# Optimization experiments

Hardware: AMD Instinct MI355X
Metric: run time of the kernel (lower is better)

The kernel has to match this reference:

```python
import jax, jax.numpy as jnp
import numpy as np

V, D_EMB, H = 50000, 200, 150
NC, NA, NT = 119, 103, 11
B, T = 32, 512
LC, LV = 50, 50
EC, EA = 600, 500


def setup_inputs() -> dict:
    key = jax.random.key(0)
    ks = iter(jax.random.split(key, 64))
    nrm = lambda shape, s=1.0: jax.random.normal(next(ks), shape, jnp.float32) * s
    rint = lambda shape, hi: jax.random.randint(next(ks), shape, 0, hi, jnp.int32)
    inp = {}
    inp['E'] = nrm((V, D_EMB), 0.1)
    inp['charge_tokens'] = rint((NC, LC), V)
    inp['article_tokens'] = rint((NA, LC), V)
    inp['documents'] = rint((B, T), V)
    inp['charge_verdict_tokens'] = rint((NC, LV), V)
    inp['article_verdict_tokens'] = rint((NA, LV), V)
    inp['c_src'] = rint((EC,), NC); inp['c_dst'] = rint((EC,), NC)
    inp['a_src'] = rint((EA,), NA); inp['a_dst'] = rint((EA,), NA)
    for nm, (i_d, h_d) in [('enc', (D_EMB, H)), ('encch', (D_EMB, H)),
                           ('term', (6 * H, 3 * H)), ('art', (8 * H, 4 * H))]:
        inp[nm + '_Wih'] = nrm((2, 3 * h_d, i_d), 1.0 / np.sqrt(i_d))
        inp[nm + '_Whh'] = nrm((2, 3 * h_d, h_d), 1.0 / np.sqrt(h_d))
        inp[nm + '_bih'] = nrm((2, 3 * h_d), 0.01)
        inp[nm + '_bhh'] = nrm((2, 3 * h_d), 0.01)
    inp['W_charge'] = nrm((NC, 6 * H), 0.05); inp['b_charge'] = nrm((NC,), 0.01)
    inp['W_article'] = nrm((NA, 8 * H), 0.05); inp['b_article'] = nrm((NA,), 0.01)
    inp['W_time'] = nrm((NT, 6 * H), 0.05); inp['b_time'] = nrm((NT,), 0.01)
    return inp


def _gru_dir(x, Wih, Whh, bih, bhh, reverse):
    # x: [B, T, I] -> outputs [B, T, H]; PyTorch GRU gate order (r, z, n)
    Bb = x.shape[0]
    Hh = Whh.shape[1]
    xs = jnp.einsum('bti,gi->btg', x, Wih) + bih  # [B,T,3H]
    if reverse:
        xs = xs[:, ::-1]
    def step(h, xt):
        gh = h @ Whh.T + bhh
        xr, xz, xn = jnp.split(xt, 3, axis=-1)
        hr, hz, hn = jnp.split(gh, 3, axis=-1)
        r = jax.nn.sigmoid(xr + hr)
        z = jax.nn.sigmoid(xz + hz)
        n = jnp.tanh(xn + r * hn)
        h = (1.0 - z) * n + z * h
        return h, h
    h0 = jnp.zeros((Bb, Hh), x.dtype)
    _, ys = jax.lax.scan(step, h0, jnp.swapaxes(xs, 0, 1))
    ys = jnp.swapaxes(ys, 0, 1)
    if reverse:
        ys = ys[:, ::-1]
    return ys


def bigru(x, Wih, Whh, bih, bhh):
    f = _gru_dir(x, Wih[0], Whh[0], bih[0], bhh[0], False)
    b = _gru_dir(x, Wih[1], Whh[1], bih[1], bhh[1], True)
    return jnp.concatenate([f, b], axis=-1)


def graph_decomp(L, src, dst, n, layers=2):
    # ragged neighbor-weighted label-graph decomposition, CSR-style via segment_sum
    counts = jax.ops.segment_sum(jnp.ones(src.shape, L.dtype), src, num_segments=n)
    for _ in range(layers):
        Li, Lj = L[src], L[dst]
        coef = (Li * Lj).sum(-1) / ((Lj * Lj).sum(-1) + 1e-10)
        agg = jax.ops.segment_sum(coef[:, None] * Lj, src, num_segments=n)
        mean = agg / jnp.maximum(counts, 1.0)[:, None]
        L = jnp.where((counts > 0)[:, None], L - mean, L)
    return L


def code_wise(query, context):
    # query [B,N,D], context [B,T,D] -> [B,D]
    S = jnp.einsum('btd,bnd->btn', context, query)
    att = jax.nn.softmax(S.max(-1), axis=-1)  # [B,T]
    return jnp.einsum('bt,btd->bd', att, context)


def mask_att(query, context):
    # query [B,Tv,D], context [B,Tc,D] -> [B,Tc,D]
    att = jnp.einsum('btd,bvd->btv', context, query)
    masked = jnp.where(att == 0, -jnp.inf, att)
    p = jax.nn.softmax(masked, axis=-1)
    p = jnp.where(jnp.isnan(p), 0.0, p)
    return jnp.einsum('btv,bvd->btd', p, query)


def fact_sep(E, verd_table, pred, enc, circumstance):
    verdict = E[verd_table[pred]]            # [B, LV, D_EMB]
    vh = bigru(verdict, *enc)                # [B, LV, 300]
    scenario = mask_att(vh, circumstance)    # [B, T, 300]
    x3 = (circumstance * scenario).sum(-1)
    x4 = (scenario * scenario).sum(-1) + 1e-10
    similar = (x3 / x4)[..., None] * scenario
    return similar, circumstance - similar


def _tile(v, t):
    return jnp.broadcast_to(v[:, None, :], (v.shape[0], t, v.shape[1]))


def reference(E, charge_tokens, article_tokens, documents, charge_verdict_tokens,
              article_verdict_tokens, c_src, c_dst, a_src, a_dst,
              enc_Wih, enc_Whh, enc_bih, enc_bhh,
              encch_Wih, encch_Whh, encch_bih, encch_bhh,
              term_Wih, term_Whh, term_bih, term_bhh,
              art_Wih, art_Whh, art_bih, art_bhh,
              W_charge, b_charge, W_article, b_article, W_time, b_time):
    enc = (enc_Wih, enc_Whh, enc_bih, enc_bhh)
    encch = (encch_Wih, encch_Whh, encch_bih, encch_bhh)
    enc_term = (term_Wih, term_Whh, term_bih, term_bhh)
    enc_art = (art_Wih, art_Whh, art_bih, art_bhh)

    ch_h = bigru(E[charge_tokens], *encch)    # [NC, LC, 300]
    ar_h = bigru(E[article_tokens], *encch)   # [NA, LC, 300]
    _charge = ch_h.mean(1)
    _article = ar_h.mean(1)
    ori_a, ori_b = _charge, _article
    new_charge = graph_decomp(_charge, c_src, c_dst, NC, 2)
    new_article = graph_decomp(_article, a_src, a_dst, NA, 2)

    d_hidden = bigru(E[documents], *enc)      # [B, T, 300]
    Bb, Tt, Dd = d_hidden.shape

    q_c = jnp.broadcast_to(new_charge[None], (Bb,) + new_charge.shape)
    d_hidden_charge = _tile(code_wise(q_c, d_hidden), Tt)
    q_a = jnp.broadcast_to(ori_a[None], (Bb,) + ori_a.shape)
    d_a = _tile(code_wise(q_a, d_hidden), Tt)

    fact_charge = jnp.concatenate([d_hidden, d_hidden_charge, d_a], -1)  # [B,T,900]
    df = fact_charge.mean(1)
    charge_out = df @ W_charge.T + b_charge

    c_pred = jnp.argmax(charge_out, axis=1)
    adc_vector, sec_vector = fact_sep(E, charge_verdict_tokens, c_pred, enc, d_hidden)

    q_na = jnp.broadcast_to(new_article[None], (Bb,) + new_article.shape)
    d_hidden_article = _tile(code_wise(q_na, d_hidden), Tt)
    q_b = jnp.broadcast_to(ori_b[None], (Bb,) + ori_b.shape)
    d_b = _tile(code_wise(q_b, d_hidden), Tt)

    fact_article = jnp.concatenate([d_hidden, d_hidden_article, adc_vector, d_b], -1)  # [B,T,1200]
    fa_h = bigru(fact_article, *enc_art)
    article_out = fa_h.mean(1) @ W_article.T + b_article

    a_pred = jnp.argmax(article_out, axis=1)
    ssc_vector, dsc_vector = fact_sep(E, article_verdict_tokens, a_pred, enc, sec_vector)

    term = jnp.concatenate([d_hidden, ssc_vector, dsc_vector], -1)  # [B,T,900]
    th = bigru(term, *enc_term)
    time_out = th.mean(1) @ W_time.T + b_time
    return (charge_out, article_out, time_out)
```

## Files before the change

### kernel.cpp

```cpp
#include <hip/hip_runtime.h>
#include <stdint.h>
#include <math.h>

typedef unsigned int u32;
typedef unsigned long long u64;
typedef _Float16 f16;
typedef _Float16 h4 __attribute__((ext_vector_type(4)));
typedef _Float16 h2 __attribute__((ext_vector_type(2)));
typedef _Float16 h8 __attribute__((ext_vector_type(8)));
typedef float f4 __attribute__((ext_vector_type(4)));

#define Vn     50000
#define DEMBn  200
#define Hn     150
#define NCn    119
#define NAn    103
#define NTn    11
#define Bn     32
#define Tn     512
#define LCn    50
#define LVn    50
#define ECn    600
#define EAn    500

#define IDIV 1073741824

__device__ __forceinline__ float sigm(float x){ return 1.0f / (1.0f + expf(-x)); }

#if __has_builtin(__builtin_amdgcn_fdot2)
__device__ __forceinline__ float FDOT2(h2 a, h2 b, float c){
  return __builtin_amdgcn_fdot2(a, b, c, false);
}
#else
__device__ __forceinline__ float FDOT2(h2 a, h2 b, float c){
  return c + (float)a.x*(float)b.x + (float)a.y*(float)b.y;
}
#endif

__device__ __forceinline__ u64 llc_load64(const u64* p){
  return __hip_atomic_load(p, __ATOMIC_RELAXED, __HIP_MEMORY_SCOPE_AGENT);
}
__device__ __forceinline__ void llc_store64(u64* p, u64 v){
  __hip_atomic_store(p, v, __ATOMIC_RELAXED, __HIP_MEMORY_SCOPE_AGENT);
}

template<int AMODE>
__global__ __launch_bounds__(256)
void gemm_k(const float* A0, const float* A1, const float* A2,
            const float* Etab, const int* tok,
            const float* Bm, int ldb, int bc0, int bc1, int bc2,
            const float* bias, const float* rowbias, int rb_div, int rb_stride,
            int arow_div, int arow_stride, int arow_off,
            float* C, int M, int N, int K)
{
  __shared__ float As[8][132];
  __shared__ float Bs[8][132];
  __shared__ int tokS[128];
  int tid = threadIdx.x;
  int m0 = blockIdx.y * 128, n0 = blockIdx.x * 128;
  if (AMODE == 1){
    for (int i = tid; i < 128; i += 256){
      int m = m0 + i;
      tokS[i] = (m < M) ? tok[m] : 0;
    }
  }
  __syncthreads();
  float acc[8][8];
  #pragma unroll
  for (int i=0;i<8;i++)
    #pragma unroll
    for (int j=0;j<8;j++) acc[i][j] = 0.f;

  int tx = tid & 15, ty = tid >> 4;

  for (int k0 = 0; k0 < K; k0 += 8){
    #pragma unroll
    for (int r = 0; r < 4; r++){
      int i = tid + 256*r;
      int ml = i >> 3, kl = i & 7;
      int k = k0 + kl;
      {
        int m = m0 + ml;
        float v = 0.f;
        if (m < M && k < K){
          if (AMODE == 0){
            int s = k / 300; int kk = k - s*300;
            const float* Ap = (s==0) ? A0 : ((s==1) ? A1 : A2);
            int ar = (m / arow_div)*arow_stride + (m % arow_div) + arow_off;
            v = Ap[(size_t)ar*300 + kk];
          } else {
            v = Etab[(size_t)tokS[ml]*DEMBn + k];
          }
        }
        As[kl][ml] = v;
      }
      {
        int n = n0 + ml;
        float v = 0.f;
        if (n < N && k < K){
          int col;
          if (AMODE == 0){ int s = k / 300; int kk = k - s*300; col = ((s==0)?bc0:((s==1)?bc1:bc2)) + kk; }
          else col = k;
          v = Bm[(size_t)n*ldb + col];
        }
        Bs[kl][ml] = v;
      }
    }
    __syncthreads();
    #pragma unroll
    for (int kk = 0; kk < 8; kk++){
      float a[8], b[8];
      #pragma unroll
      for (int i=0;i<8;i++) a[i] = As[kk][ty*8+i];
      #pragma unroll
      for (int i=0;i<8;i++) b[i] = Bs[kk][tx*8+i];
      #pragma unroll
      for (int i=0;i<8;i++)
        #pragma unroll
        for (int j=0;j<8;j++) acc[i][j] += a[i]*b[j];
    }
    __syncthreads();
  }
  #pragma unroll
  for (int i=0;i<8;i++){
    int m = m0 + ty*8 + i; if (m >= M) continue;
    #pragma unroll
    for (int j=0;j<8;j++){
      int n = n0 + tx*8 + j; if (n >= N) continue;
      float v = acc[i][j];
      if (bias)    v += bias[n];
      if (rowbias) v += rowbias[(size_t)(m / rb_div)*rb_stride + n];
      C[(size_t)m*N + n] = v;
    }
  }
}

__global__ __launch_bounds__(256)
void score_rowmax_k(const float* A, const float* Bq, int Nq, float* RMX)
{
  __shared__ float As[8][132];
  __shared__ float Bs[8][132];
  int tid = threadIdx.x;
  int m0 = blockIdx.x * 128;
  float acc[8][8];
  #pragma unroll
  for (int i=0;i<8;i++)
    #pragma unroll
    for (int j=0;j<8;j++) acc[i][j] = 0.f;
  int tx = tid & 15, ty = tid >> 4;

  for (int k0 = 0; k0 < 300; k0 += 8){
    #pragma unroll
    for (int r = 0; r < 4; r++){
      int i = tid + 256*r;
      int ml = i >> 3, kl = i & 7;
      int k = k0 + kl;
      As[kl][ml] = (k < 300) ? A[(size_t)(m0 + ml)*300 + k] : 0.f;
      Bs[kl][ml] = (ml < Nq && k < 300) ? Bq[(size_t)ml*300 + k] : 0.f;
    }
    __syncthreads();
    #pragma unroll
    for (int kk = 0; kk < 8; kk++){
      float a[8], b[8];
      #pragma unroll
      for (int i=0;i<8;i++) a[i] = As[kk][ty*8+i];
      #pragma unroll
      for (int i=0;i<8;i++) b[i] = Bs[kk][tx*8+i];
      #pragma unroll
      for (int i=0;i<8;i++)
        #pragma unroll
        for (int j=0;j<8;j++) acc[i][j] += a[i]*b[j];
    }
    __syncthreads();
  }
  #pragma unroll
  for (int i=0;i<8;i++){
    float mx = -INFINITY;
    #pragma unroll
    for (int j=0;j<8;j++){
      int n = tx*8 + j;
      if (n < Nq) mx = fmaxf(mx, acc[i][j]);
    }
    mx = fmaxf(mx, __shfl_xor(mx, 1));
    mx = fmaxf(mx, __shfl_xor(mx, 2));
    mx = fmaxf(mx, __shfl_xor(mx, 4));
    mx = fmaxf(mx, __shfl_xor(mx, 8));
    if (tx == 0) RMX[m0 + ty*8 + i] = mx;
  }
}

__global__ __launch_bounds__(256)
void stage_mfma_k(const float* A0, const float* A1, const float* A2,
                  const float* Bm, int ldb, int bc0, int bc1, int bc2,
                  const float* bias, const float* rowbias, int rb_stride,
                  int arow_off,
                  float* C, int N, int K)
{
  constexpr int KP = 40;
  __shared__ __align__(16) f16 Ah[128*KP];
  __shared__ __align__(16) f16 Al[128*KP];
  __shared__ __align__(16) f16 Bh[128*KP];
  __shared__ __align__(16) f16 Bl[128*KP];

  int tid = threadIdx.x;
  int n0 = blockIdx.x * 128, m0 = blockIdx.y * 128;
  int lane = tid & 63, w = tid >> 6;
  int wr = (w >> 1) * 64, wc = (w & 1) * 64;
  int li = lane & 15, lk = (lane >> 4) * 8;

  f4 acc[4][4];
  #pragma unroll
  for (int i=0;i<4;i++)
    #pragma unroll
    for (int j=0;j<4;j++) acc[i][j] = (f4){0.f,0.f,0.f,0.f};

  int srow = tid >> 1, scb = (tid & 1) << 4;
  int sm = m0 + srow;
  size_t abase = (size_t)(((sm >> 8) * 512) + (sm & 255) + arow_off) * 300;
  int sn = n0 + srow;

  for (int k0 = 0; k0 < K; k0 += 32){
    #pragma unroll
    for (int q = 0; q < 16; q += 2){
      float2 va = {0.f, 0.f}, vb = {0.f, 0.f};
      int k = k0 + scb + q;
      if (k < K){
        int s = (k >= 600) ? 2 : ((k >= 300) ? 1 : 0);
        int kk = k - s*300;
        const float* Ap = (s==0) ? A0 : ((s==1) ? A1 : A2);
        va = *(const float2*)&Ap[abase + kk];
        if (sn < N) vb = *(const float2*)&Bm[(size_t)sn*ldb + ((s==0)?bc0:((s==1)?bc1:bc2)) + kk];
      }
      f16 a0h=(f16)va.x, a1h=(f16)va.y, b0h=(f16)vb.x, b1h=(f16)vb.y;
      f16 a0l=(f16)(va.x-(float)a0h), a1l=(f16)(va.y-(float)a1h);
      f16 b0l=(f16)(vb.x-(float)b0h), b1l=(f16)(vb.y-(float)b1h);
      int off = srow*KP + scb + q;
      *(h2*)&Ah[off] = (h2){a0h, a1h};
      *(h2*)&Al[off] = (h2){a0l, a1l};
      *(h2*)&Bh[off] = (h2){b0h, b1h};
      *(h2*)&Bl[off] = (h2){b0l, b1l};
    }
    __syncthreads();

    h8 fah[4], fal[4], fbh[4], fbl[4];
    #pragma unroll
    for (int f = 0; f < 4; f++){
      fah[f] = *(const h8*)&Ah[(wr + f*16 + li)*KP + lk];
      fal[f] = *(const h8*)&Al[(wr + f*16 + li)*KP + lk];
      fbh[f] = *(const h8*)&Bh[(wc + f*16 + li)*KP + lk];
      fbl[f] = *(const h8*)&Bl[(wc + f*16 + li)*KP + lk];
    }
    #pragma unroll
    for (int i = 0; i < 4; i++)
      #pragma unroll
      for (int j = 0; j < 4; j++){
        acc[i][j] = __builtin_amdgcn_mfma_f32_16x16x32_f16(fah[i], fbh[j], acc[i][j], 0,0,0);
        acc[i][j] = __builtin_amdgcn_mfma_f32_16x16x32_f16(fah[i], fbl[j], acc[i][j], 0,0,0);
        acc[i][j] = __builtin_amdgcn_mfma_f32_16x16x32_f16(fal[i], fbh[j], acc[i][j], 0,0,0);
      }
    __syncthreads();
  }

  #pragma unroll
  for (int i = 0; i < 4; i++){
    int r0 = m0 + wr + i*16 + (lane >> 4)*4;
    #pragma unroll
    for (int j = 0; j < 4; j++){
      int c = n0 + wc + j*16 + li;
      if (c < N){
        float badd = bias ? bias[c] : 0.f;
        #pragma unroll
        for (int r = 0; r < 4; r++){
          int row = r0 + r;
          float v = acc[i][j][r] + badd;
          if (rowbias) v += rowbias[(size_t)(row >> 8)*rb_stride + c];
          C[(size_t)row*N + c] = v;
        }
      }
    }
  }
}

__global__ __launch_bounds__(256)
void embed_mfma_k(const float* Etab, const int* tok,
                  const float* Bm, const float* bias,
                  float* C, int M, int N, int K)
{
  constexpr int KP = 40;
  __shared__ __align__(16) f16 Ah[128*KP];
  __shared__ __align__(16) f16 Al[128*KP];
  __shared__ __align__(16) f16 Bh[128*KP];
  __shared__ __align__(16) f16 Bl[128*KP];
  __shared__ int tokS[128];

  int tid = threadIdx.x;
  int n0 = blockIdx.x * 128, m0 = blockIdx.y * 128;
  int lane = tid & 63, w = tid >> 6;
  int wr = (w >> 1) * 64, wc = (w & 1) * 64;
  int li = lane & 15, lk = (lane >> 4) * 8;

  for (int i = tid; i < 128; i += 256){
    int m = m0 + i;
    tokS[i] = (m < M) ? tok[m] : 0;
  }
  __syncthreads();

  f4 acc[4][4];
  #pragma unroll
  for (int i=0;i<4;i++)
    #pragma unroll
    for (int j=0;j<4;j++) acc[i][j] = (f4){0.f,0.f,0.f,0.f};

  int srow = tid >> 1, scb = (tid & 1) << 4;
  size_t abase = (size_t)tokS[srow] * (size_t)K;
  int sn = n0 + srow;

  for (int k0 = 0; k0 < K; k0 += 32){
    #pragma unroll
    for (int q = 0; q < 16; q += 2){
      float2 va = {0.f, 0.f}, vb = {0.f, 0.f};
      int k = k0 + scb + q;
      if (k < K){
        va = *(const float2*)&Etab[abase + k];
        if (sn < N) vb = *(const float2*)&Bm[(size_t)sn*K + k];
      }
      f16 a0h=(f16)va.x, a1h=(f16)va.y, b0h=(f16)vb.x, b1h=(f16)vb.y;
      f16 a0l=(f16)(va.x-(float)a0h), a1l=(f16)(va.y-(float)a1h);
      f16 b0l=(f16)(vb.x-(float)b0h), b1l=(f16)(vb.y-(float)b1h);
      int off = srow*KP + scb + q;
      *(h2*)&Ah[off] = (h2){a0h, a1h};
      *(h2*)&Al[off] = (h2){a0l, a1l};
      *(h2*)&Bh[off] = (h2){b0h, b1h};
      *(h2*)&Bl[off] = (h2){b0l, b1l};
    }
    __syncthreads();

    h8 fah[4], fal[4], fbh[4], fbl[4];
    #pragma unroll
    for (int f = 0; f < 4; f++){
      fah[f] = *(const h8*)&Ah[(wr + f*16 + li)*KP + lk];
      fal[f] = *(const h8*)&Al[(wr + f*16 + li)*KP + lk];
      fbh[f] = *(const h8*)&Bh[(wc + f*16 + li)*KP + lk];
      fbl[f] = *(const h8*)&Bl[(wc + f*16 + li)*KP + lk];
    }
    #pragma unroll
    for (int i = 0; i < 4; i++)
      #pragma unroll
      for (int j = 0; j < 4; j++){
        acc[i][j] = __builtin_amdgcn_mfma_f32_16x16x32_f16(fah[i], fbh[j], acc[i][j], 0,0,0);
        acc[i][j] = __builtin_amdgcn_mfma_f32_16x16x32_f16(fah[i], fbl[j], acc[i][j], 0,0,0);
        acc[i][j] = __builtin_amdgcn_mfma_f32_16x16x32_f16(fal[i], fbh[j], acc[i][j], 0,0,0);
      }
    __syncthreads();
  }

  #pragma unroll
  for (int i = 0; i < 4; i++){
    int r0 = m0 + wr + i*16 + (lane >> 4)*4;
    #pragma unroll
    for (int j = 0; j < 4; j++){
      int c = n0 + wc + j*16 + li;
      if (c < N){
        float badd = bias ? bias[c] : 0.f;
        #pragma unroll
        for (int r = 0; r < 4; r++){
          int row = r0 + r;
          if (row < M) C[(size_t)row*N + c] = acc[i][j][r] + badd;
        }
      }
    }
  }
}

__global__ __launch_bounds__(640)
void gru_small_k(const float* xs, int ncols,
                 const float* Whh, const float* bhh,
                 float* ys, float* meanOut, int T)
{
  constexpr int KSTEP = 38;
  __shared__ __align__(16) float hl[2][152];
  int tid = threadIdx.x;
  int seq = blockIdx.x, dir = blockIdx.y;
  int row = tid >> 2, l = tid & 3;
  bool comp = (row < 150);
  int k0 = l * KSTEP;

  float w0[KSTEP], w1[KSTEP], w2[KSTEP];
  if (comp){
    const float* base = Whh + (size_t)dir*67500;
    const float* p0 = base + (size_t)(0*150 + row)*150;
    const float* p1 = base + (size_t)(1*150 + row)*150;
    const float* p2 = base + (size_t)(2*150 + row)*150;
    #pragma unroll
    for (int i=0;i<KSTEP;i++){
      int k = k0 + i;
      int kc = (k < 150) ? k : 0;
      float m = (k < 150) ? 1.f : 0.f;
      w0[i] = p0[kc]*m; w1[i] = p1[kc]*m; w2[i] = p2[kc]*m;
    }
  }
  float bR=0.f, bZ=0.f, bN=0.f;
  if (comp && l==0){
    bR = bhh[dir*450 + row];
    bZ = bhh[dir*450 + 150 + row];
    bN = bhh[dir*450 + 300 + row];
  }
  for (int i = tid; i < 2*152; i += 640) (&hl[0][0])[i] = 0.f;
  __syncthreads();

  float msum = 0.f;
  size_t rowbase = (size_t)seq * T;
  for (int tt = 0; tt < T; tt++){
    int t = dir ? (T-1-tt) : tt;
    int par = tt & 1;
    const float* hr = hl[par];
    float* hw = hl[1-par];

    float xr=0.f, xz=0.f, xn=0.f, hprev=0.f;
    if (comp && l==0){
      const float* xp = xs + (rowbase + t)*(size_t)ncols + dir*450;
      xr = xp[row]; xz = xp[150+row]; xn = xp[300+row];
      hprev = hr[row];
    }

    float a0=0.f, a1=0.f, a2=0.f;
    if (comp){
      #pragma unroll
      for (int i=0;i<KSTEP;i++){
        float hv = hr[k0 + i];
        a0 += w0[i]*hv; a1 += w1[i]*hv; a2 += w2[i]*hv;
      }
    }
    a0 += __shfl_xor(a0,1); a0 += __shfl_xor(a0,2);
    a1 += __shfl_xor(a1,1); a1 += __shfl_xor(a1,2);
    a2 += __shfl_xor(a2,1); a2 += __shfl_xor(a2,2);

    if (comp && l==0){
      float rr = sigm(xr + a0 + bR);
      float zz = sigm(xz + a1 + bZ);
      float nn = tanhf(xn + rr*(a2 + bN));
      float hn = (1.f - zz)*nn + zz*hprev;
      hw[row] = hn;
      msum += hn;
      if (ys) ys[(rowbase + t)*(size_t)300 + dir*150 + row] = hn;
    }
    __syncthreads();
  }
  if (meanOut && comp && l==0)
    meanOut[(size_t)seq*300 + dir*150 + row] = msum / (float)T;
}

template<int BLK, int JB, int KC, int Hh>
__global__ __launch_bounds__(BLK)
void gru_big_k(const float* xs0, const float* xs1,
               const float* Whh,
               const float* bhh,
               u64* hbuf,
               float* hseed,
               float* meanOut, int mean_stride,
               u32 tagbase,
               int TT, int TC, int t0)
{
  constexpr int LPR   = 8;
  constexpr int KSTEP = 2*KC;
  constexpr int HS    = LPR*KSTEP;
  constexpr int HP    = Hh/2;
  constexpr int NPAIR = 4*HP;
  constexpr int RMAX  = (NPAIR + BLK - 1)/BLK;
  constexpr int H3    = 3*Hh;

  __shared__ __align__(16) f16 hstage[2][4*HS];

  int tid = threadIdx.x;
  int jc = blockIdx.x, bg = blockIdx.y, dir = blockIdx.z;
  int j0 = jc * JB;
  int row = tid >> 3, l = tid & 7;
  bool comp = (row < JB);
  int jg = j0 + row;
  int k0 = l * KSTEP;

  const float* Wd = Whh + (size_t)dir*H3*Hh;
  const float* xs = dir ? xs1 : xs0;
  int xoff = dir ? (TT - TC - t0) : t0;

  h2 w0[KC], w1[KC], w2[KC];
  if (comp){
    const float* p0 = Wd + ((size_t)0*Hh + jg)*(size_t)Hh;
    const float* p1 = Wd + ((size_t)1*Hh + jg)*(size_t)Hh;
    const float* p2 = Wd + ((size_t)2*Hh + jg)*(size_t)Hh;
    #pragma unroll
    for (int i=0;i<KC;i++){
      int k = k0 + 2*i;
      h2 a; a.x=(f16)0.f; a.y=(f16)0.f;
      h2 b = a, c = a;
      if (k < Hh){   a.x=(f16)p0[k];   b.x=(f16)p1[k];   c.x=(f16)p2[k]; }
      if (k+1 < Hh){ a.y=(f16)p0[k+1]; b.y=(f16)p1[k+1]; c.y=(f16)p2[k+1]; }
      w0[i]=a; w1[i]=b; w2[i]=c;
    }
  } else {
    #pragma unroll
    for (int i=0;i<KC;i++){
      h2 z; z.x=(f16)0.f; z.y=(f16)0.f;
      w0[i]=z; w1[i]=z; w2[i]=z;
    }
  }
  float br=0.f, bz=0.f, bn_=0.f;
  if (comp && l < 4){
    br = bhh[(size_t)dir*H3 + jg];
    bz = bhh[(size_t)dir*H3 + Hh + jg];
    bn_= bhh[(size_t)dir*H3 + 2*Hh + jg];
  }

  {
    f16* hz = &hstage[0][0];
    for (int i = tid; i < 2*4*HS; i += BLK) hz[i] = (f16)0.f;
  }

  float msum_own = 0.f;
  float hold_own = 0.f;
  if (t0 > 0 && comp && l < 4){
    const float* hs = hseed + (size_t)dir*Bn*Hh;
    hold_own = hs[(size_t)(bg*4+l)*Hh + jg];
  }
  __syncthreads();

  for (int tt = 0; tt < TC; tt++){
    int g = t0 + tt;
    int t = dir ? (TT-1-g) : g;
    int par = g & 1;
    const u64* hrd = hbuf + (size_t)(par*2 + dir)*Bn*HP;
    u64*       hwr = hbuf + (size_t)((1-par)*2 + dir)*Bn*HP;
    f16* hsb = hstage[par];

    u64 tmp[RMAX];
    const u64* hb = hrd + (size_t)(bg*4)*HP;
    if (g != 0){
      #pragma unroll
      for (int r=0;r<RMAX;r++){
        int idx = tid + r*BLK;
        if (idx < NPAIR) tmp[r] = llc_load64(&hb[idx]);
      }
    }

    float xr=0.f, xz=0.f, xn=0.f;
    if (comp && l < 4){
      const float* xp = xs + ((size_t)(bg*4+l)*TC + (t - xoff))*(size_t)H3;
      xr = xp[jg]; xz = xp[Hh+jg]; xn = xp[2*Hh+jg];
    }

    if (g != 0){
      u32 want = tagbase + (u32)g;
      u32 pend = 0;
      #pragma unroll
      for (int r=0;r<RMAX;r++){
        int idx = tid + r*BLK;
        if (idx < NPAIR && (u32)(tmp[r] >> 32) != want) pend |= (1u << r);
      }
      int guard = 0;
      while (pend){
        __builtin_amdgcn_s_sleep(1);
        #pragma unroll
        for (int r=0;r<RMAX;r++)
          if (pend & (1u << r)) tmp[r] = llc_load64(&hb[tid + r*BLK]);
        #pragma unroll
        for (int r=0;r<RMAX;r++)
          if ((pend & (1u << r)) && (u32)(tmp[r] >> 32) == want) pend &= ~(1u << r);
        if (++guard > 200000) break;
      }
      #pragma unroll
      for (int r=0;r<RMAX;r++){
        int idx = tid + r*BLK;
        if (idx < NPAIR){
          int s = idx / HP, jp = idx - s*HP;
          union { u32 i; h2 h; } u; u.i = (u32)tmp[r];
          *(h2*)(hsb + s*HS + 2*jp) = u.h;
        }
      }
    }
    __syncthreads();

    float a0[4]={0,0,0,0}, a1[4]={0,0,0,0}, a2[4]={0,0,0,0};
    if (comp){
      const f16* hp = hsb + k0;
      #pragma unroll
      for (int i=0;i<KC;i++){
        const int kk = 2*i;
        h2 hv0 = *(const h2*)(hp + 0*HS + kk);
        h2 hv1 = *(const h2*)(hp + 1*HS + kk);
        h2 hv2 = *(const h2*)(hp + 2*HS + kk);
        h2 hv3 = *(const h2*)(hp + 3*HS + kk);
        a0[0]=FDOT2(w0[i],hv0,a0[0]); a0[1]=FDOT2(w0[i],hv1,a0[1]);
        a0[2]=FDOT2(w0[i],hv2,a0[2]); a0[3]=FDOT2(w0[i],hv3,a0[3]);
        a1[0]=FDOT2(w1[i],hv0,a1[0]); a1[1]=FDOT2(w1[i],hv1,a1[1]);
        a1[2]=FDOT2(w1[i],hv2,a1[2]); a1[3]=FDOT2(w1[i],hv3,a1[3]);
        a2[0]=FDOT2(w2[i],hv0,a2[0]); a2[1]=FDOT2(w2[i],hv1,a2[1]);
        a2[2]=FDOT2(w2[i],hv2,a2[2]); a2[3]=FDOT2(w2[i],hv3,a2[3]);
      }
    }
    #pragma unroll
    for (int s=0;s<4;s++){
      a0[s] += __shfl_xor(a0[s],1); a0[s] += __shfl_xor(a0[s],2); a0[s] += __shfl_xor(a0[s],4);
      a1[s] += __shfl_xor(a1[s],1); a1[s] += __shfl_xor(a1[s],2); a1[s] += __shfl_xor(a1[s],4);
      a2[s] += __shfl_xor(a2[s],1); a2[s] += __shfl_xor(a2[s],2); a2[s] += __shfl_xor(a2[s],4);
    }
    float t0a = (l & 1) ? a0[1] : a0[0], t0b = (l & 1) ? a0[3] : a0[2];
    float A0 = (l & 2) ? t0b : t0a;
    float t1a = (l & 1) ? a1[1] : a1[0], t1b = (l & 1) ? a1[3] : a1[2];
    float A1 = (l & 2) ? t1b : t1a;
    float t2a = (l & 1) ? a2[1] : a2[0], t2b = (l & 1) ? a2[3] : a2[2];
    float A2 = (l & 2) ? t2b : t2a;

    float hn_own = 0.f;
    if (comp && l < 4){
      float rr = sigm(xr + A0 + br);
      float zz = sigm(xz + A1 + bz);
      float nn = tanhf(xn + rr*(A2 + bn_));
      hn_own = (1.f - zz)*nn + zz*hold_own;
      hold_own = hn_own;
      msum_own += hn_own;
    }
    u32 wtag = tagbase + (u32)g + 1u;
    float hp2 = __shfl_down(hn_own, 8);
    if (comp && l < 4 && !(row & 1)){
      h2 pk; pk.x = (f16)hn_own; pk.y = (f16)hp2;
      union { h2 h; u32 i; } u; u.h = pk;
      llc_store64(&hwr[(size_t)(bg*4+l)*HP + ((unsigned)(j0+row) >> 1)],
                  ((u64)wtag << 32) | (u64)u.i);
    }
    if (tt == TC-1 && comp && l < 4){
      float* hs = hseed + (size_t)dir*Bn*Hh;
      hs[(size_t)(bg*4+l)*Hh + jg] = hold_own;
    }
  }
  if (comp && l < 4){
    float* mp = meanOut + (size_t)(bg*4+l)*mean_stride + dir*Hh + jg;
    *mp += msum_own / (float)TT;
  }
}

__global__ __launch_bounds__(256)
void mask_att_k(const float* ctx, const float* vh, float* simOut, float* diffOut)
{
  __shared__ __align__(16) float vhl[50*300];
  __shared__ __align__(16) float ctxl[8*300];
  __shared__ float attl[8*52];
  __shared__ __align__(16) float scenl[8*300];
  __shared__ float ratio[8];
  int tid = threadIdx.x;
  int b = blockIdx.y, tc = blockIdx.x;
  int grp = tid >> 5, ln = tid & 31;
  size_t cbase = ((size_t)b*Tn + tc*8) * 300;
  {
    const f4* vsrc = (const f4*)(vh + (size_t)b*15000);
    f4* vdst = (f4*)vhl;
    for (int i = tid; i < 3750; i += 256) vdst[i] = vsrc[i];
    const f4* csrc = (const f4*)(ctx + cbase);
    f4* cdst = (f4*)ctxl;
    for (int i = tid; i < 600; i += 256) cdst[i] = csrc[i];
  }
  __syncthreads();
  for (int p = tid; p < 400; p += 256){
    int ttl = p / 50, v = p % 50;
    const f4* cp = (const f4*)(ctxl + ttl*300);
    const f4* vp = (const f4*)(vhl + v*300);
    float acc = 0.f;
    for (int d4 = 0; d4 < 75; d4++){
      f4 c = cp[d4], vv = vp[d4];
      acc += c.x*vv.x + c.y*vv.y + c.z*vv.z + c.w*vv.w;
    }
    attl[ttl*52 + v] = acc;
  }
  __syncthreads();
  {
    float mx = -INFINITY;
    for (int v = ln; v < 50; v += 32){
      float a = attl[grp*52+v];
      float msk = (a == 0.f) ? -INFINITY : a;
      attl[grp*52+v] = msk;
      mx = fmaxf(mx, msk);
    }
    #pragma unroll
    for (int m=1; m<32; m<<=1) mx = fmaxf(mx, __shfl_xor(mx, m));
    if (mx == -INFINITY){
      for (int v = ln; v < 50; v += 32) attl[grp*52+v] = 0.f;
    } else {
      float sum = 0.f;
      for (int v = ln; v < 50; v += 32){
        float e = expf(attl[grp*52+v] - mx);
        attl[grp*52+v] = e;
        sum += e;
      }
      #pragma unroll
      for (int m=1; m<32; m<<=1) sum += __shfl_xor(sum, m);
      float inv = 1.f/sum;
      for (int v = ln; v < 50; v += 32) attl[grp*52+v] *= inv;
    }
  }
  __syncthreads();
  for (int p = tid; p < 2400; p += 256){
    int ttl = p / 300, d = p % 300;
    float acc = 0.f;
    for (int v=0; v<50; v++) acc += attl[ttl*52+v] * vhl[v*300+d];
    scenl[p] = acc;
  }
  __syncthreads();
  {
    float x3 = 0.f, x4 = 0.f;
    for (int d = ln; d < 300; d += 32){
      float s = scenl[grp*300+d];
      x3 += ctxl[grp*300+d]*s; x4 += s*s;
    }
    #pragma unroll
    for (int m=1; m<32; m<<=1){ x3 += __shfl_xor(x3, m); x4 += __shfl_xor(x4, m); }
    if (ln == 0) ratio[grp] = x3 / (x4 + 1e-10f);
  }
  __syncthreads();
  {
    f4* so = (f4*)(simOut + cbase);
    f4* dfo = (f4*)(diffOut + cbase);
    const f4* sc = (const f4*)scenl;
    const f4* cl = (const f4*)ctxl;
    for (int p4 = tid; p4 < 600; p4 += 256){
      float rt = ratio[p4 / 75];
      f4 s = sc[p4], c = cl[p4];
      f4 sim = (f4){rt*s.x, rt*s.y, rt*s.z, rt*s.w};
      so[p4] = sim;
      dfo[p4] = (f4){c.x - sim.x, c.y - sim.y, c.z - sim.z, c.w - sim.w};
    }
  }
}

__global__ __launch_bounds__(256)
void softmaxT_k(const float* m, float* att){
  __shared__ float red[256];
  int b = blockIdx.x, tid = threadIdx.x;
  float v1 = m[b*512 + tid], v2 = m[b*512 + 256 + tid];
  red[tid] = fmaxf(v1, v2); __syncthreads();
  for (int s=128; s; s>>=1){ if (tid<s) red[tid] = fmaxf(red[tid], red[tid+s]); __syncthreads(); }
  float M = red[0]; __syncthreads();
  float e1 = expf(v1-M), e2 = expf(v2-M);
  red[tid] = e1+e2; __syncthreads();
  for (int s=128; s; s>>=1){ if (tid<s) red[tid] += red[tid+s]; __syncthreads(); }
  float inv = 1.f / red[0];
  att[b*512+tid] = e1*inv; att[b*512+256+tid] = e2*inv;
}

__global__ __launch_bounds__(256)
void wsum_k(const float* att, const float* dh, float* out){
  int b = blockIdx.x, c = blockIdx.y, tid = threadIdx.x;
  int t0 = c * 64;
  for (int d = tid; d < 300; d += 256){
    float acc = 0.f;
    #pragma unroll 8
    for (int t = t0; t < t0 + 64; t++)
      acc += att[b*512+t] * dh[((size_t)b*512 + t)*300 + d];
    atomicAdd(&out[b*300+d], acc);
  }
}

__global__ void count_k(const int* src, int E, float* counts){
  int e = blockIdx.x*256 + threadIdx.x;
  if (e < E) atomicAdd(&counts[src[e]], 1.f);
}
__global__ void coef_k(const float* L, const int* src, const int* dst, int E, float* coef){
  int e = blockIdx.x*4 + (threadIdx.x >> 6);
  int lane = threadIdx.x & 63;
  if (e >= E) return;
  const float* Li = L + (size_t)src[e]*300;
  const float* Lj = L + (size_t)dst[e]*300;
  float num = 0.f, den = 0.f;
  for (int d = lane; d < 300; d += 64){ float lj = Lj[d]; num += Li[d]*lj; den += lj*lj; }
  for (int off = 32; off; off >>= 1){ num += __shfl_xor(num, off, 64); den += __shfl_xor(den, off, 64); }
  if (lane == 0) coef[e] = num / (den + 1e-10f);
}
__global__ void agg_k(const float* L, const int* src, const int* dst, const float* coef, int E, float* agg){
  int e = blockIdx.x;
  float c = coef[e];
  const float* Lj = L + (size_t)dst[e]*300;
  float* ag = agg + (size_t)src[e]*300;
  for (int d = threadIdx.x; d < 300; d += 256) atomicAdd(&ag[d], c*Lj[d]);
}
__global__ void upd_k(const float* L, const float* agg, const float* counts, float* out, int n){
  int i = blockIdx.x;
  float c = counts[i];
  for (int d = threadIdx.x; d < 300; d += 256){
    float v = L[(size_t)i*300+d];
    out[(size_t)i*300+d] = (c > 0.f) ? v - agg[(size_t)i*300+d]/fmaxf(c, 1.f) : v;
  }
}

__global__ __launch_bounds__(256)
void logits_k(const float* A0, const float* A1, const float* A2, int srcw,
              const float* W, const float* bias, int C, int K,
              float* outF){
  int b = blockIdx.x;
  int c = blockIdx.y*4 + (threadIdx.x >> 6);
  int lane = threadIdx.x & 63;
  if (c >= C) return;
  const float* wp = W + (size_t)c*K;
  float acc = 0.f;
  for (int k = lane; k < K; k += 64){
    int s = k / srcw; int kk = k - s*srcw;
    const float* Ap = (s==0) ? A0 : ((s==1) ? A1 : A2);
    acc += Ap[(size_t)b*srcw + kk] * wp[k];
  }
  for (int off = 32; off; off >>= 1) acc += __shfl_xor(acc, off, 64);
  if (lane == 0) outF[b*C + c] = acc + bias[c];
}
__global__ void argmax_k(const float* lf, int C, int* pred){
  int b = threadIdx.x;
  if (b < 32){
    const float* p = lf + (size_t)b*C;
    int best = 0; float bv = p[0];
    for (int c = 1; c < C; c++){ float v = p[c]; if (v > bv){ bv = v; best = c; } }
    pred[b] = best;
  }
}
__global__ void vtok_k(const int* table, const int* pred, int* vt, int L){
  int i = blockIdx.x*256 + threadIdx.x;
  if (i < 32*L) vt[i] = table[pred[i/L]*L + i%L];
}

extern "C" void kernel_launch(void* const* d_in, const int* in_sizes, int n_in,
                              void* d_out, int out_size, void* d_ws, size_t ws_size,
                              hipStream_t stream)
{
  (void)in_sizes; (void)n_in; (void)out_size;
  const float* E        = (const float*)d_in[0];
  const int* chTok    = (const int*)d_in[1];
  const int* arTok    = (const int*)d_in[2];
  const int* docs     = (const int*)d_in[3];
  const int* chVerd   = (const int*)d_in[4];
  const int* arVerd   = (const int*)d_in[5];
  const int* c_src    = (const int*)d_in[6];
  const int* c_dst    = (const int*)d_in[7];
  const int* a_src    = (const int*)d_in[8];
  const int* a_dst    = (const int*)d_in[9];
  const float* enc_Wih  = (const float*)d_in[10];
  const float* enc_Whh  = (const float*)d_in[11];
  const float* enc_bih  = (const float*)d_in[12];
  const float* enc_bhh  = (const float*)d_in[13];
  const float* ech_Wih  = (const float*)d_in[14];
  const float* ech_Whh  = (const float*)d_in[15];
  const float* ech_bih  = (const float*)d_in[16];
  const float* ech_bhh  = (const float*)d_in[17];
  const float* term_Wih = (const float*)d_in[18];
  const float* term_Whh = (const float*)d_in[19];
  const float* term_bih = (const float*)d_in[20];
  const float* term_bhh = (const float*)d_in[21];
  const float* art_Wih  = (const float*)d_in[22];
  const float* art_Whh  = (const float*)d_in[23];
  const float* art_bih  = (const float*)d_in[24];
  const float* art_bhh  = (const float*)d_in[25];
  const float* W_charge = (const float*)d_in[26];
  const float* b_charge = (const float*)d_in[27];
  const float* W_article= (const float*)d_in[28];
  const float* b_article= (const float*)d_in[29];
  const float* W_time   = (const float*)d_in[30];
  const float* b_time   = (const float*)d_in[31];
  float* out = (float*)d_out;
  float* OUTC = out;
  float* OUTA = out + 3808;
  float* OUTT = out + 7104;

  char* wsb = (char*)d_ws;
  size_t off = 0;
  auto alloc = [&](size_t nf)->float* {
    float* p = (float*)(wsb + off);
    off += ((nf*4 + 255) & ~(size_t)255);
    return p;
  };
  float* XS0   = alloc(14745600ULL);
  float* XS1   = alloc(14745600ULL);
  float* DH    = alloc(4915200);
  float* ADC   = alloc(4915200);
  float* SEC   = alloc(4915200);
  float* SSC   = alloc(4915200);
  float* VHYS  = alloc(480000);
  float* MECH  = alloc(66600);
  float* LC1   = alloc(35700);
  float* LC0   = alloc(35700);
  float* LA1   = alloc(30900);
  float* LA0   = alloc(30900);
  float* AGG   = alloc(35700);
  float* CNTS  = alloc(256);
  float* COEF  = alloc(640);
  float* DHC   = alloc(9600);
  float* DA    = alloc(9600);
  float* DHNA  = alloc(9600);
  float* DB    = alloc(9600);
  float* MDH   = alloc(9600);
  float* MFA   = alloc(38400);
  float* MTH   = alloc(28800);
  float* RB    = alloc(115200);
  float* RMX   = alloc(16384);
  float* ATTB  = alloc(16384);
  u64*   HBUF  = (u64*)alloc(76800);
  float* HSEED = alloc(38400);
  int*   PREDC = (int*)alloc(64);
  int*   PREDA = (int*)alloc(64);
  int*   VTOK  = (int*)alloc(1600);
  int*   TCC   = (int*)alloc(11104);

  if (off > ws_size) return;

  hipMemsetAsync(HBUF, 0, 2*2*Bn*300*sizeof(u64), stream);
  hipMemsetAsync(CNTS, 0, 256*4, stream);
  hipMemsetAsync(DHC, 0, 4*9600*4, stream);

  hipMemcpyAsync(TCC, chTok, NCn*LCn*4, hipMemcpyDeviceToDevice, stream);
  hipMemcpyAsync(TCC + NCn*LCn, arTok, NAn*LCn*4, hipMemcpyDeviceToDevice, stream);
  embed_mfma_k<<<dim3(8,87),256,0,stream>>>(E, TCC, ech_Wih, ech_bih,
      XS0, 11100, 900, 200);
  gru_small_k<<<dim3(222,2),640,0,stream>>>(XS0, 900, ech_Whh, ech_bhh, nullptr, MECH, 50);

  embed_mfma_k<<<dim3(8,128),256,0,stream>>>(E, docs, enc_Wih, enc_bih,
      XS0, 16384, 900, 200);
  gru_small_k<<<dim3(32,2),640,0,stream>>>(XS0, 900, enc_Whh, enc_bhh, DH, MDH, 512);

  count_k<<<3,256,0,stream>>>(c_src, ECn, CNTS);
  count_k<<<2,256,0,stream>>>(a_src, EAn, CNTS+128);
  coef_k<<<150,256,0,stream>>>(MECH, c_src, c_dst, ECn, COEF);
  hipMemsetAsync(AGG, 0, 35700*4, stream);
  agg_k<<<ECn,256,0,stream>>>(MECH, c_src, c_dst, COEF, ECn, AGG);
  upd_k<<<NCn,256,0,stream>>>(MECH, AGG, CNTS, LC1, NCn);
  coef_k<<<150,256,0,stream>>>(LC1, c_src, c_dst, ECn, COEF);
  hipMemsetAsync(AGG, 0, 35700*4, stream);
  agg_k<<<ECn,256,0,stream>>>(LC1, c_src, c_dst, COEF, ECn, AGG);
  upd_k<<<NCn,256,0,stream>>>(LC1, AGG, CNTS, LC0, NCn);

  const float* MEAR = MECH + (size_t)NCn*300;
  coef_k<<<125,256,0,stream>>>(MEAR, a_src, a_dst, EAn, COEF);
  hipMemsetAsync(AGG, 0, 30900*4, stream);
  agg_k<<<EAn,256,0,stream>>>(MEAR, a_src, a_dst, COEF, EAn, AGG);
  upd_k<<<NAn,256,0,stream>>>(MEAR, AGG, CNTS+128, LA1, NAn);
  coef_k<<<125,256,0,stream>>>(LA1, a_src, a_dst, EAn, COEF);
  hipMemsetAsync(AGG, 0, 30900*4, stream);
  agg_k<<<EAn,256,0,stream>>>(LA1, a_src, a_dst, COEF, EAn, AGG);
  upd_k<<<NAn,256,0,stream>>>(LA1, AGG, CNTS+128, LA0, NAn);

  auto codewise = [&](const float* q, int Nq, float* outv){
    score_rowmax_k<<<128,256,0,stream>>>(DH, q, Nq, RMX);
    softmaxT_k<<<32,256,0,stream>>>(RMX, ATTB);
    wsum_k<<<dim3(32,8),256,0,stream>>>(ATTB, DH, outv);
  };
  codewise(LC0,  NCn, DHC);
  codewise(MECH, NCn, DA);
  codewise(LA0,  NAn, DHNA);
  codewise(MEAR, NAn, DB);

  logits_k<<<dim3(32,30),256,0,stream>>>(MDH, DHC, DA, 300, W_charge, b_charge, NCn, 900, OUTC);
  argmax_k<<<1,64,0,stream>>>(OUTC, NCn, PREDC);

  vtok_k<<<7,256,0,stream>>>(chVerd, PREDC, VTOK, LVn);
  embed_mfma_k<<<dim3(8,13),256,0,stream>>>(E, VTOK, enc_Wih, enc_bih,
      XS0, 1600, 900, 200);
  gru_small_k<<<dim3(32,2),640,0,stream>>>(XS0, 900, enc_Whh, enc_bhh, VHYS, nullptr, 50);
  mask_att_k<<<dim3(64,32),256,0,stream>>>(DH, VHYS, ADC, SEC);

  {
    dim3 g((3600+127)/128, 1);
    gemm_k<0><<<g,256,0,stream>>>(DHNA, DB, nullptr, nullptr, nullptr,
        art_Wih, 1200, 300, 900, 0, art_bih, nullptr, 1, 1, IDIV,0,0,
        RB, 32, 3600, 600);
  }
  hipMemsetAsync(MFA, 0, 38400*4, stream);
  for (int L = 0; L < 2; L++){
    stage_mfma_k<<<dim3(15,64),256,0,stream>>>(DH, ADC, nullptr,
        art_Wih, 1200, 0, 600, 0,
        nullptr, RB, 3600, 256*L,
        XS0, 1800, 600);
    stage_mfma_k<<<dim3(15,64),256,0,stream>>>(DH, ADC, nullptr,
        art_Wih + (size_t)1800*1200, 1200, 0, 600, 0,
        nullptr, RB + 1800, 3600, 256*(1-L),
        XS1, 1800, 600);
    gru_big_k<384,40,38,600><<<dim3(15,8,2),384,0,stream>>>(XS0, XS1,
        art_Whh, art_bhh, HBUF, HSEED, MFA, 1200, 0u,
        512, 256, 256*L);
  }
  logits_k<<<dim3(32,26),256,0,stream>>>(MFA, nullptr, nullptr, 1200, W_article, b_article, NAn, 1200, OUTA);
  argmax_k<<<1,64,0,stream>>>(OUTA, NAn, PREDA);

  vtok_k<<<7,256,0,stream>>>(arVerd, PREDA, VTOK, LVn);
  embed_mfma_k<<<dim3(8,13),256,0,stream>>>(E, VTOK, enc_Wih, enc_bih,
      XS0, 1600, 900, 200);
  gru_small_k<<<dim3(32,2),640,0,stream>>>(XS0, 900, enc_Whh, enc_bhh, VHYS, nullptr, 50);
  mask_att_k<<<dim3(64,32),256,0,stream>>>(SEC, VHYS, SSC, ADC);

  hipMemsetAsync(MTH, 0, 28800*4, stream);
  for (int L = 0; L < 2; L++){
    stage_mfma_k<<<dim3(11,64),256,0,stream>>>(DH, SSC, ADC,
        term_Wih, 900, 0, 300, 600,
        term_bih, nullptr, 0, 256*L,
        XS0, 1350, 900);
    stage_mfma_k<<<dim3(11,64),256,0,stream>>>(DH, SSC, ADC,
        term_Wih + (size_t)1350*900, 900, 0, 300, 600,
        term_bih + 1350, nullptr, 0, 256*(1-L),
        XS1, 1350, 900);
    gru_big_k<448,50,29,450><<<dim3(9,8,2),448,0,stream>>>(XS0, XS1,
        term_Whh, term_bhh, HBUF, HSEED, MTH, 900, 512u,
        512, 256, 256*L);
  }
  logits_k<<<dim3(32,3),256,0,stream>>>(MTH, nullptr, nullptr, 900, W_time, b_time, NTn, 900, OUTT);
}
```

Before: 9.457 ms.

## Batch four codewise attention passes into single launches and remap MFMA blocks per XCD

The four codewise score/softmax/weighted-sum sequences now run as one launch each, with a grid dimension selecting the query set. This cuts launch count and raises parallelism per launch. The stage MFMA kernel remaps block indices so that each XCD gets a contiguous range of M rows, aiming for better L2 reuse. The mask attention scenario loop is also vectorised to float4. The batched wsum relies on the four output buffers being contiguous in memory.

```diff
diff --git a/kernel.cpp b/kernel.cpp
--- a/kernel.cpp
+++ b/kernel.cpp
@@ -136,12 +136,18 @@
 }
 
 __global__ __launch_bounds__(256)
-void score_rowmax_k(const float* A, const float* Bq, int Nq, float* RMX)
+void score_rowmax_k(const float* A,
+                    const float* B0, const float* B1,
+                    const float* B2, const float* B3,
+                    int Nq01, int Nq23, float* RMX)
 {
   __shared__ float As[8][132];
   __shared__ float Bs[8][132];
   int tid = threadIdx.x;
   int m0 = blockIdx.x * 128;
+  int qi = blockIdx.y;
+  const float* Bq = (qi==0) ? B0 : ((qi==1) ? B1 : ((qi==2) ? B2 : B3));
+  int Nq = (qi < 2) ? Nq01 : Nq23;
   float acc[8][8];
   #pragma unroll
   for (int i=0;i<8;i++)
@@ -185,7 +191,7 @@
     mx = fmaxf(mx, __shfl_xor(mx, 2));
     mx = fmaxf(mx, __shfl_xor(mx, 4));
     mx = fmaxf(mx, __shfl_xor(mx, 8));
-    if (tx == 0) RMX[m0 + ty*8 + i] = mx;
+    if (tx == 0) RMX[(size_t)qi*16384 + m0 + ty*8 + i] = mx;
   }
 }
 
@@ -203,7 +209,19 @@
   __shared__ __align__(16) f16 Bl[128*KP];
 
   int tid = threadIdx.x;
-  int n0 = blockIdx.x * 128, m0 = blockIdx.y * 128;
+  int nb, mb;
+  if ((gridDim.y & 7) == 0){
+    int bid = blockIdx.y * gridDim.x + blockIdx.x;
+    int xcd = bid & 7;
+    int i = bid >> 3;
+    int NB = gridDim.x;
+    nb = i % NB;
+    int mlocal = i / NB;
+    mb = xcd * (gridDim.y >> 3) + mlocal;
+  } else {
+    nb = blockIdx.x; mb = blockIdx.y;
+  }
+  int n0 = nb * 128, m0 = mb * 128;
   int lane = tid & 63, w = tid >> 6;
   int wr = (w >> 1) * 64, wc = (w & 1) * 64;
   int li = lane & 15, lk = (lane >> 4) * 8;
@@ -697,11 +715,15 @@
     }
   }
   __syncthreads();
-  for (int p = tid; p < 2400; p += 256){
-    int ttl = p / 300, d = p % 300;
-    float acc = 0.f;
-    for (int v=0; v<50; v++) acc += attl[ttl*52+v] * vhl[v*300+d];
-    scenl[p] = acc;
+  for (int p4 = tid; p4 < 600; p4 += 256){
+    int ttl = p4 / 75, d4 = p4 % 75;
+    f4 acc = (f4){0.f,0.f,0.f,0.f};
+    for (int v = 0; v < 50; v++){
+      float a = attl[ttl*52+v];
+      f4 vv = ((const f4*)(vhl + v*300))[d4];
+      acc.x += a*vv.x; acc.y += a*vv.y; acc.z += a*vv.z; acc.w += a*vv.w;
+    }
+    ((f4*)scenl)[p4] = acc;
   }
   __syncthreads();
   {
@@ -734,7 +756,8 @@
 void softmaxT_k(const float* m, float* att){
   __shared__ float red[256];
   int b = blockIdx.x, tid = threadIdx.x;
-  float v1 = m[b*512 + tid], v2 = m[b*512 + 256 + tid];
+  size_t base = (size_t)blockIdx.y*16384;
+  float v1 = m[base + b*512 + tid], v2 = m[base + b*512 + 256 + tid];
   red[tid] = fmaxf(v1, v2); __syncthreads();
   for (int s=128; s; s>>=1){ if (tid<s) red[tid] = fmaxf(red[tid], red[tid+s]); __syncthreads(); }
   float M = red[0]; __syncthreads();
@@ -742,19 +765,22 @@
   red[tid] = e1+e2; __syncthreads();
   for (int s=128; s; s>>=1){ if (tid<s) red[tid] += red[tid+s]; __syncthreads(); }
   float inv = 1.f / red[0];
-  att[b*512+tid] = e1*inv; att[b*512+256+tid] = e2*inv;
+  att[base + b*512+tid] = e1*inv; att[base + b*512+256+tid] = e2*inv;
 }
 
 __global__ __launch_bounds__(256)
 void wsum_k(const float* att, const float* dh, float* out){
   int b = blockIdx.x, c = blockIdx.y, tid = threadIdx.x;
+  int qi = blockIdx.z;
+  const float* ap = att + (size_t)qi*16384 + b*512;
+  float* op = out + (size_t)qi*9600 + b*300;
   int t0 = c * 64;
   for (int d = tid; d < 300; d += 256){
     float acc = 0.f;
     #pragma unroll 8
     for (int t = t0; t < t0 + 64; t++)
-      acc += att[b*512+t] * dh[((size_t)b*512 + t)*300 + d];
-    atomicAdd(&out[b*300+d], acc);
+      acc += ap[t] * dh[((size_t)b*512 + t)*300 + d];
+    atomicAdd(&op[d], acc);
   }
 }
 
@@ -893,8 +919,8 @@
   float* MFA   = alloc(38400);
   float* MTH   = alloc(28800);
   float* RB    = alloc(115200);
-  float* RMX   = alloc(16384);
-  float* ATTB  = alloc(16384);
+  float* RMX   = alloc(65536);
+  float* ATTB  = alloc(65536);
   u64*   HBUF  = (u64*)alloc(76800);
   float* HSEED = alloc(38400);
   int*   PREDC = (int*)alloc(64);
@@ -939,15 +965,10 @@
   agg_k<<<EAn,256,0,stream>>>(LA1, a_src, a_dst, COEF, EAn, AGG);
   upd_k<<<NAn,256,0,stream>>>(LA1, AGG, CNTS+128, LA0, NAn);
 
-  auto codewise = [&](const float* q, int Nq, float* outv){
-    score_rowmax_k<<<128,256,0,stream>>>(DH, q, Nq, RMX);
-    softmaxT_k<<<32,256,0,stream>>>(RMX, ATTB);
-    wsum_k<<<dim3(32,8),256,0,stream>>>(ATTB, DH, outv);
-  };
-  codewise(LC0,  NCn, DHC);
-  codewise(MECH, NCn, DA);
-  codewise(LA0,  NAn, DHNA);
-  codewise(MEAR, NAn, DB);
+  score_rowmax_k<<<dim3(128,4),256,0,stream>>>(DH, LC0, MECH, LA0, MEAR,
+      NCn, NAn, RMX);
+  softmaxT_k<<<dim3(32,4),256,0,stream>>>(RMX, ATTB);
+  wsum_k<<<dim3(32,8,4),256,0,stream>>>(ATTB, DH, DHC);
 
   logits_k<<<dim3(32,30),256,0,stream>>>(MDH, DHC, DA, 300, W_charge, b_charge, NCn, 900, OUTC);
   argmax_k<<<1,64,0,stream>>>(OUTC, NCn, PREDC);
```

Result: faster. 8.952 ms (-5.3%).
